# Kernel tuning notes

Measured on AMD Instinct MI355X. Metric: run time of the kernel, lower is better.

## Reference

```python
import jax, jax.numpy as jnp
import numpy as np

DEPTH = 9
NUM_LEAVES = 2 ** DEPTH            # 512
NUM_BRANCHES = 2 ** DEPTH - 1      # 511


def _leaf_paths(depth):
    """For each leaf, the BFS (heap-order) branch indices along its root->leaf
    path and the left/right bit taken at each branch (1 = right)."""
    L = 2 ** depth
    idx = np.zeros((L, depth), np.int32)
    bits = np.zeros((L, depth), np.int32)
    for l in range(L):
        node = 0
        for t in range(depth):
            b = (l >> (depth - 1 - t)) & 1
            idx[l, t] = node
            bits[l, t] = b
            node = 2 * node + 1 + b
    return jnp.asarray(idx), jnp.asarray(bits)

PATH_IDX, PATH_BITS = _leaf_paths(DEPTH)


def setup_inputs() -> dict:
    key = jax.random.key(0)
    k1, k2, k3 = jax.random.split(key, 3)
    B, D, W, H = 128, 256, 28, 28
    C = 200
    return {
        "xs": jax.random.normal(k1, (B, D, W, H), jnp.float32),
        "prototypes": jax.random.normal(k2, (NUM_BRANCHES, D, 1, 1), jnp.float32),
        "leaf_params": jax.random.normal(k3, (NUM_LEAVES, C), jnp.float32),
    }


def reference(xs, prototypes, leaf_params):
    # ---- L2Conv2D: squared-L2 distance map via conv decomposition ----
    B, D, W, H = xs.shape
    P = prototypes.shape[0]
    p = prototypes.reshape(P, D)                       # W1 = H1 = 1
    x2 = jnp.sum(xs * xs, axis=1)                      # [B, W, H]
    p2 = jnp.sum(p * p, axis=1)                        # [P]
    xp = jnp.einsum('bdwh,pd->bpwh', xs, p)            # [B, P, W, H]
    sq = x2[:, None] - 2.0 * xp + p2[None, :, None, None]
    distances = jnp.sqrt(jnp.abs(sq) + 1e-14)          # [B, P, W, H]

    # ---- min-pool over full spatial extent (avg-pool unused: focal off) ----
    min_distances = jnp.min(distances, axis=(2, 3))    # [B, P]
    similarities = jnp.exp(-min_distances)             # [B, P], ps per branch

    # ---- soft tree routing: pa(leaf) = prod over path of ps / (1-ps) ----
    ps_path = similarities[:, PATH_IDX]                # [B, L, depth]
    step = jnp.where(PATH_BITS[None] == 1, ps_path, 1.0 - ps_path)
    pa = jnp.prod(step, axis=-1)                       # [B, L]

    # ---- mix leaf class distributions (distributed sampling strategy) ----
    ds = jax.nn.softmax(leaf_params, axis=-1)          # [L, C]
    return pa @ ds                                     # [B, C]
```

## Files before the change

kernel.cpp:

```cpp
#include <hip/hip_runtime.h>
#include <hip/hip_bf16.h>

typedef __attribute__((ext_vector_type(8))) short bf16x8;
typedef __attribute__((ext_vector_type(4))) float f32x4;

#define D_K    256
#define WH     784
#define WHH    392
#define P_REAL 511
#define P_PAD  512
#define C_OUT  200
#define NLEAF  512
#define TDEPTH 9

#define NT      32
#define NTILES  13
#define TILE_USH 8192

#define WS_PB   0
#define WS_P2   262144
#define WS_DS   264192
#define WS_PM   673792

static __device__ __forceinline__ unsigned short f2bf(float x) {
    union { float f; unsigned int u; } v; v.f = x;
    unsigned int r = v.u + 0x7FFFu + ((v.u >> 16) & 1u);
    return (unsigned short)(r >> 16);
}

__global__ __launch_bounds__(64)
void prep2_kernel(const float* __restrict__ protos, const float* __restrict__ lp,
                  unsigned short* __restrict__ pb, float* __restrict__ p2,
                  float* __restrict__ ds) {
    int bid = blockIdx.x;
    int l = threadIdx.x;
    if (bid < P_PAD) {
        int p = bid;
        f32x4 v = {0.f, 0.f, 0.f, 0.f};
        if (p < P_REAL)
            v = *reinterpret_cast<const f32x4*>(protos + (size_t)p * D_K + 4 * l);
        ushort4 w;
        w.x = f2bf(-2.f * v[0]); w.y = f2bf(-2.f * v[1]);
        w.z = f2bf(-2.f * v[2]); w.w = f2bf(-2.f * v[3]);
        *reinterpret_cast<ushort4*>(pb + (size_t)p * D_K + 4 * l) = w;
        float s = v[0]*v[0] + v[1]*v[1] + v[2]*v[2] + v[3]*v[3];
#pragma unroll
        for (int m = 32; m >= 1; m >>= 1) s += __shfl_xor(s, m, 64);
        if (l == 0) p2[p] = s;
    } else {
        int row = bid - P_PAD;
        float v[4];
        float mx = -3.4e38f;
#pragma unroll
        for (int i = 0; i < 4; ++i) {
            int c = l + 64 * i;
            v[i] = (c < C_OUT) ? lp[(size_t)row * C_OUT + c] : -3.4e38f;
            mx = fmaxf(mx, v[i]);
        }
#pragma unroll
        for (int m = 32; m >= 1; m >>= 1) mx = fmaxf(mx, __shfl_xor(mx, m, 64));
        float sum = 0.f;
#pragma unroll
        for (int i = 0; i < 4; ++i) {
            int c = l + 64 * i;
            if (c < C_OUT) { v[i] = expf(v[i] - mx); sum += v[i]; }
        }
#pragma unroll
        for (int m = 32; m >= 1; m >>= 1) sum += __shfl_xor(sum, m, 64);
        float inv = 1.f / sum;
#pragma unroll
        for (int i = 0; i < 4; ++i) {
            int c = l + 64 * i;
            if (c < C_OUT) ds[(size_t)row * C_OUT + c] = v[i] * inv;
        }
    }
}

__global__ __launch_bounds__(512, 2)
void proto_min_kernel(const float* __restrict__ xs,
                      const unsigned short* __restrict__ pb,
                      float* __restrict__ pm) {
    __shared__ unsigned short Xs[2][TILE_USH];
    __shared__ float x2buf[2][8*68 + 8];

    const int tid  = threadIdx.x;
    const int wv   = tid >> 6;
    const int lane = tid & 63;
    const int g    = lane >> 4;
    const int lr   = lane & 15;

    const int b   = blockIdx.x >> 1;
    const int whh = blockIdx.x & 1;

    const float* xb = xs + (size_t)b * (D_K * WH) + whh * WHH;

    bf16x8 af[4][8];
#pragma unroll
    for (int mf = 0; mf < 4; ++mf) {
        const unsigned short* rp = pb + (size_t)(64*wv + 16*mf + lr) * D_K + 8*g;
#pragma unroll
        for (int ks = 0; ks < 8; ++ks)
            af[mf][ks] = *reinterpret_cast<const bf16x8*>(rp + 32*ks);
    }

    const int n4 = tid & 7;
    const int kq = tid >> 3;

    float rmin[4][4];
#pragma unroll
    for (int mf = 0; mf < 4; ++mf)
#pragma unroll
        for (int r = 0; r < 4; ++r) rmin[mf][r] = 3.0e38f;

    f32x4 ld[4];

#define LOAD_TILE(T) do {                                                     \
        int colb = (T) * NT + 4 * n4;                                         \
        if (colb > WHH - 4) colb = WHH - 4;                                   \
        const float* rowp = xb + (size_t)(4*kq) * WH + colb;                  \
        _Pragma("unroll")                                                     \
        for (int r = 0; r < 4; ++r)                                           \
            ld[r] = *reinterpret_cast<const f32x4*>(rowp + r * WH);           \
    } while (0)

#define STAGE_TILE(DST) do {                                                  \
        f32x4 x2a = {0.f, 0.f, 0.f, 0.f};                                     \
        _Pragma("unroll")                                                     \
        for (int r = 0; r < 4; ++r) {                                         \
            f32x4 v = ld[r];                                                  \
            x2a[0] += v[0]*v[0]; x2a[1] += v[1]*v[1];                         \
            x2a[2] += v[2]*v[2]; x2a[3] += v[3]*v[3];                         \
        }                                                                     \
        _Pragma("unroll")                                                     \
        for (int c = 0; c < 4; ++c) {                                         \
            int n = 4*n4 + c;                                                 \
            float2 f01 = make_float2(ld[0][c], ld[1][c]);                     \
            float2 f23 = make_float2(ld[2][c], ld[3][c]);                     \
            __hip_bfloat162 b01 = __float22bfloat162_rn(f01);                 \
            __hip_bfloat162 b23 = __float22bfloat162_rn(f23);                 \
            uint2 w;                                                          \
            w.x = *reinterpret_cast<unsigned int*>(&b01);                     \
            w.y = *reinterpret_cast<unsigned int*>(&b23);                     \
            int off = n*256 + (((kq >> 1) ^ (n & 7)) << 3) + ((kq & 1) << 2); \
            *reinterpret_cast<uint2*>(&Xs[DST][off]) = w;                     \
        }                                                                     \
        _Pragma("unroll")                                                     \
        for (int c = 0; c < 4; ++c) {                                         \
            x2a[c] += __shfl_xor(x2a[c], 8, 64);                              \
            x2a[c] += __shfl_xor(x2a[c], 16, 64);                             \
            x2a[c] += __shfl_xor(x2a[c], 32, 64);                             \
        }                                                                     \
        if (lane < 8) {                                                       \
            _Pragma("unroll")                                                 \
            for (int c = 0; c < 4; ++c)                                       \
                x2buf[DST][lane*68 + c*8 + wv] = x2a[c];                      \
        }                                                                     \
    } while (0)

#define X2_READ(NF, OUT) do {                                                 \
        int n = 16*(NF) + lr;                                                 \
        const float* xp = &x2buf[buf][(n >> 2)*68 + (n & 3)*8];               \
        f32x4 q0 = *reinterpret_cast<const f32x4*>(xp);                       \
        f32x4 q1 = *reinterpret_cast<const f32x4*>(xp + 4);                   \
        OUT = ((q0[0]+q0[1]) + (q0[2]+q0[3]))                                 \
            + ((q1[0]+q1[1]) + (q1[2]+q1[3]));                                \
    } while (0)

#define BURST(NF, ACC) do {                                                   \
        __builtin_amdgcn_s_setprio(1);                                        \
        _Pragma("unroll")                                                     \
        for (int ks = 0; ks < 8; ++ks) {                                      \
            int n = 16*(NF) + lr;                                             \
            int off = n*256 + ((((ks << 2) + g) ^ (n & 7)) << 3);             \
            bf16x8 bfr = *reinterpret_cast<const bf16x8*>(&Xs[buf][off]);     \
            _Pragma("unroll")                                                 \
            for (int mf = 0; mf < 4; ++mf)                                    \
                ACC[mf] = __builtin_amdgcn_mfma_f32_16x16x32_bf16(            \
                    af[mf][ks], bfr, ACC[mf], 0, 0, 0);                       \
        }                                                                     \
        __builtin_amdgcn_s_setprio(0);                                        \
    } while (0)

#define MIN_UPD(ACC) do {                                                     \
        _Pragma("unroll")                                                     \
        for (int mf = 0; mf < 4; ++mf)                                        \
            _Pragma("unroll")                                                 \
            for (int r = 0; r < 4; ++r)                                       \
                rmin[mf][r] = fminf(rmin[mf][r], ACC[mf][r]);                 \
    } while (0)

    LOAD_TILE(0);
    STAGE_TILE(0);
    __syncthreads();

    int buf = 0;
    f32x4 acc0[4], acc1[4];

    for (int t = 0; t < NTILES - 1; ++t) {
        LOAD_TILE(t + 1);

        float x2v0; X2_READ(0, x2v0);
#pragma unroll
        for (int mf = 0; mf < 4; ++mf)
            acc0[mf] = (f32x4){x2v0, x2v0, x2v0, x2v0};

        BURST(0, acc0);
        MIN_UPD(acc0);

        STAGE_TILE(buf ^ 1);

        float x2v1; X2_READ(1, x2v1);
#pragma unroll
        for (int mf = 0; mf < 4; ++mf)
            acc1[mf] = (f32x4){x2v1, x2v1, x2v1, x2v1};

        BURST(1, acc1);
        MIN_UPD(acc1);

        __syncthreads();
        buf ^= 1;
    }

    {
        float x2v0; X2_READ(0, x2v0);
#pragma unroll
        for (int mf = 0; mf < 4; ++mf)
            acc0[mf] = (f32x4){x2v0, x2v0, x2v0, x2v0};
        BURST(0, acc0);
        MIN_UPD(acc0);

        float x2v1; X2_READ(1, x2v1);
#pragma unroll
        for (int mf = 0; mf < 4; ++mf)
            acc1[mf] = (f32x4){x2v1, x2v1, x2v1, x2v1};
        BURST(1, acc1);
        MIN_UPD(acc1);
    }

#pragma unroll
    for (int mf = 0; mf < 4; ++mf)
#pragma unroll
        for (int r = 0; r < 4; ++r) {
            float v = rmin[mf][r];
#pragma unroll
            for (int m = 1; m <= 8; m <<= 1)
                v = fminf(v, __shfl_xor(v, m, 64));
            rmin[mf][r] = v;
        }

    if (lr == 0) {
        float* pmw = pm + ((size_t)b * 2 + whh) * P_PAD;
#pragma unroll
        for (int mf = 0; mf < 4; ++mf)
#pragma unroll
            for (int r = 0; r < 4; ++r)
                pmw[64*wv + 16*mf + 4*g + r] = rmin[mf][r];
    }
#undef LOAD_TILE
#undef STAGE_TILE
#undef X2_READ
#undef BURST
#undef MIN_UPD
}

__global__ __launch_bounds__(256)
void out_kernel(const float* __restrict__ pm, const float* __restrict__ p2,
                const float* __restrict__ ds, float* __restrict__ out) {
    __shared__ float sim[NLEAF];
    __shared__ float pa[NLEAF];
    int b = blockIdx.x;
    int t = threadIdx.x;
    const float* pm0 = pm + (size_t)b * 2 * P_PAD;
#pragma unroll
    for (int j = 0; j < 2; ++j) {
        int p = t + 256 * j;
        float m = fminf(pm0[p], pm0[P_PAD + p]);
        float sq = m + p2[p];
        sim[p] = expf(-sqrtf(fabsf(sq) + 1e-14f));
    }
    __syncthreads();
#pragma unroll
    for (int j = 0; j < 2; ++j) {
        int leaf = t + 256 * j;
        int node = 0;
        float prod = 1.f;
#pragma unroll
        for (int st = 0; st < TDEPTH; ++st) {
            int bit = (leaf >> (TDEPTH - 1 - st)) & 1;
            float sv = sim[node];
            prod *= bit ? sv : (1.f - sv);
            node = 2 * node + 1 + bit;
        }
        pa[leaf] = prod;
    }
    __syncthreads();
    if (t < C_OUT) {
        float a0 = 0.f, a1 = 0.f, a2 = 0.f, a3 = 0.f;
        for (int l = 0; l < NLEAF; l += 4) {
            a0 += pa[l + 0] * ds[(size_t)(l + 0) * C_OUT + t];
            a1 += pa[l + 1] * ds[(size_t)(l + 1) * C_OUT + t];
            a2 += pa[l + 2] * ds[(size_t)(l + 2) * C_OUT + t];
            a3 += pa[l + 3] * ds[(size_t)(l + 3) * C_OUT + t];
        }
        out[(size_t)b * C_OUT + t] = (a0 + a1) + (a2 + a3);
    }
}

extern "C" void kernel_launch(void* const* d_in, const int* in_sizes, int n_in,
                              void* d_out, int out_size, void* d_ws, size_t ws_size,
                              hipStream_t stream) {
    (void)in_sizes; (void)n_in; (void)out_size; (void)ws_size;
    const float* xs     = (const float*)d_in[0];
    const float* protos = (const float*)d_in[1];
    const float* lp     = (const float*)d_in[2];
    float* out = (float*)d_out;

    char* ws = (char*)d_ws;
    unsigned short* pb = (unsigned short*)(ws + WS_PB);
    float* p2   = (float*)(ws + WS_P2);
    float* dsm  = (float*)(ws + WS_DS);
    float* pm   = (float*)(ws + WS_PM);

    prep2_kernel<<<1024, 64, 0, stream>>>(protos, lp, pb, p2, dsm);
    proto_min_kernel<<<256, 512, 0, stream>>>(xs, pb, pm);
    out_kernel<<<128, 256, 0, stream>>>(pm, p2, dsm, out);
}
```

Baseline: 58.47 us.

## Deepen global-load prefetch to two tiles ahead and change LDS swizzle key

Replaces the single register staging buffer with two (ldA/ldB) so global loads for tile t+2/t+3 are issued two tiles ahead of use. The main loop is unrolled by two so the LDS buffer indices are compile-time constants. It also changes the XOR swizzle key for the bf16 tile in shared memory to (n ^ n>>2)&7, aiming to reduce bank conflicts on stores and reads. The deeper prefetch hides more global-memory latency at the cost of extra VGPRs, which may lower occupancy.

```diff
diff --git a/kernel.cpp b/kernel.cpp
--- a/kernel.cpp
+++ b/kernel.cpp
@@ -112,36 +112,37 @@
 #pragma unroll
         for (int r = 0; r < 4; ++r) rmin[mf][r] = 3.0e38f;
 
-    f32x4 ld[4];
-
-#define LOAD_TILE(T) do {                                                     \
+    f32x4 ldA[4], ldB[4];
+
+#define LOAD_T(T, LD) do {                                                    \
         int colb = (T) * NT + 4 * n4;                                         \
         if (colb > WHH - 4) colb = WHH - 4;                                   \
         const float* rowp = xb + (size_t)(4*kq) * WH + colb;                  \
         _Pragma("unroll")                                                     \
         for (int r = 0; r < 4; ++r)                                           \
-            ld[r] = *reinterpret_cast<const f32x4*>(rowp + r * WH);           \
-    } while (0)
-
-#define STAGE_TILE(DST) do {                                                  \
+            LD[r] = *reinterpret_cast<const f32x4*>(rowp + r * WH);           \
+    } while (0)
+
+#define STAGE_T(DST, LD) do {                                                 \
         f32x4 x2a = {0.f, 0.f, 0.f, 0.f};                                     \
         _Pragma("unroll")                                                     \
         for (int r = 0; r < 4; ++r) {                                         \
-            f32x4 v = ld[r];                                                  \
+            f32x4 v = LD[r];                                                  \
             x2a[0] += v[0]*v[0]; x2a[1] += v[1]*v[1];                         \
             x2a[2] += v[2]*v[2]; x2a[3] += v[3]*v[3];                         \
         }                                                                     \
         _Pragma("unroll")                                                     \
         for (int c = 0; c < 4; ++c) {                                         \
             int n = 4*n4 + c;                                                 \
-            float2 f01 = make_float2(ld[0][c], ld[1][c]);                     \
-            float2 f23 = make_float2(ld[2][c], ld[3][c]);                     \
+            int key = (n ^ n4) & 7;                                           \
+            float2 f01 = make_float2(LD[0][c], LD[1][c]);                     \
+            float2 f23 = make_float2(LD[2][c], LD[3][c]);                     \
             __hip_bfloat162 b01 = __float22bfloat162_rn(f01);                 \
             __hip_bfloat162 b23 = __float22bfloat162_rn(f23);                 \
             uint2 w;                                                          \
             w.x = *reinterpret_cast<unsigned int*>(&b01);                     \
             w.y = *reinterpret_cast<unsigned int*>(&b23);                     \
-            int off = n*256 + (((kq >> 1) ^ (n & 7)) << 3) + ((kq & 1) << 2); \
+            int off = n*256 + (((kq >> 1) ^ key) << 3) + ((kq & 1) << 2);     \
             *reinterpret_cast<uint2*>(&Xs[DST][off]) = w;                     \
         }                                                                     \
         _Pragma("unroll")                                                     \
@@ -157,22 +158,23 @@
         }                                                                     \
     } while (0)
 
-#define X2_READ(NF, OUT) do {                                                 \
+#define X2_READ(BUF, NF, OUT) do {                                            \
         int n = 16*(NF) + lr;                                                 \
-        const float* xp = &x2buf[buf][(n >> 2)*68 + (n & 3)*8];               \
+        const float* xp = &x2buf[BUF][(n >> 2)*68 + (n & 3)*8];               \
         f32x4 q0 = *reinterpret_cast<const f32x4*>(xp);                       \
         f32x4 q1 = *reinterpret_cast<const f32x4*>(xp + 4);                   \
         OUT = ((q0[0]+q0[1]) + (q0[2]+q0[3]))                                 \
             + ((q1[0]+q1[1]) + (q1[2]+q1[3]));                                \
     } while (0)
 
-#define BURST(NF, ACC) do {                                                   \
+#define BURST(BUF, NF, ACC) do {                                              \
         __builtin_amdgcn_s_setprio(1);                                        \
         _Pragma("unroll")                                                     \
         for (int ks = 0; ks < 8; ++ks) {                                      \
             int n = 16*(NF) + lr;                                             \
-            int off = n*256 + ((((ks << 2) + g) ^ (n & 7)) << 3);             \
-            bf16x8 bfr = *reinterpret_cast<const bf16x8*>(&Xs[buf][off]);     \
+            int key = (n ^ (n >> 2)) & 7;                                     \
+            int off = n*256 + (((((ks) << 2) + g) ^ key) << 3);               \
+            bf16x8 bfr = *reinterpret_cast<const bf16x8*>(&Xs[BUF][off]);     \
             _Pragma("unroll")                                                 \
             for (int mf = 0; mf < 4; ++mf)                                    \
                 ACC[mf] = __builtin_amdgcn_mfma_f32_16x16x32_bf16(            \
@@ -189,52 +191,51 @@
                 rmin[mf][r] = fminf(rmin[mf][r], ACC[mf][r]);                 \
     } while (0)
 
-    LOAD_TILE(0);
-    STAGE_TILE(0);
+#define TILE_BODY(T, CUR, NXT, LD) do {                                       \
+        f32x4 acc[4];                                                         \
+        float x2v0; X2_READ(CUR, 0, x2v0);                                    \
+        _Pragma("unroll")                                                     \
+        for (int mf = 0; mf < 4; ++mf)                                        \
+            acc[mf] = (f32x4){x2v0, x2v0, x2v0, x2v0};                        \
+        BURST(CUR, 0, acc);                                                   \
+        MIN_UPD(acc);                                                         \
+        STAGE_T(NXT, LD);                                                     \
+        if ((T) + 3 < NTILES) LOAD_T((T) + 3, LD);                            \
+        float x2v1; X2_READ(CUR, 1, x2v1);                                    \
+        _Pragma("unroll")                                                     \
+        for (int mf = 0; mf < 4; ++mf)                                        \
+            acc[mf] = (f32x4){x2v1, x2v1, x2v1, x2v1};                        \
+        BURST(CUR, 1, acc);                                                   \
+        MIN_UPD(acc);                                                         \
+        __syncthreads();                                                      \
+    } while (0)
+
+    LOAD_T(0, ldA);
+    STAGE_T(0, ldA);
+    LOAD_T(1, ldA);
+    LOAD_T(2, ldB);
     __syncthreads();
 
-    int buf = 0;
-    f32x4 acc0[4], acc1[4];
-
-    for (int t = 0; t < NTILES - 1; ++t) {
-        LOAD_TILE(t + 1);
-
-        float x2v0; X2_READ(0, x2v0);
+    for (int tt = 0; tt < 6; ++tt) {
+        const int t0 = 2 * tt;
+        TILE_BODY(t0,     0, 1, ldA);
+        TILE_BODY(t0 + 1, 1, 0, ldB);
+    }
+
+    {
+        f32x4 acc[4];
+        float x2v0; X2_READ(0, 0, x2v0);
 #pragma unroll
         for (int mf = 0; mf < 4; ++mf)
-            acc0[mf] = (f32x4){x2v0, x2v0, x2v0, x2v0};
-
-        BURST(0, acc0);
-        MIN_UPD(acc0);
-
-        STAGE_TILE(buf ^ 1);
-
-        float x2v1; X2_READ(1, x2v1);
+            acc[mf] = (f32x4){x2v0, x2v0, x2v0, x2v0};
+        BURST(0, 0, acc);
+        MIN_UPD(acc);
+        float x2v1; X2_READ(0, 1, x2v1);
 #pragma unroll
         for (int mf = 0; mf < 4; ++mf)
-            acc1[mf] = (f32x4){x2v1, x2v1, x2v1, x2v1};
-
-        BURST(1, acc1);
-        MIN_UPD(acc1);
-
-        __syncthreads();
-        buf ^= 1;
-    }
-
-    {
-        float x2v0; X2_READ(0, x2v0);
-#pragma unroll
-        for (int mf = 0; mf < 4; ++mf)
-            acc0[mf] = (f32x4){x2v0, x2v0, x2v0, x2v0};
-        BURST(0, acc0);
-        MIN_UPD(acc0);
-
-        float x2v1; X2_READ(1, x2v1);
-#pragma unroll
-        for (int mf = 0; mf < 4; ++mf)
-            acc1[mf] = (f32x4){x2v1, x2v1, x2v1, x2v1};
-        BURST(1, acc1);
-        MIN_UPD(acc1);
+            acc[mf] = (f32x4){x2v1, x2v1, x2v1, x2v1};
+        BURST(0, 1, acc);
+        MIN_UPD(acc);
     }
 
 #pragma unroll
@@ -256,11 +257,12 @@
             for (int r = 0; r < 4; ++r)
                 pmw[64*wv + 16*mf + 4*g + r] = rmin[mf][r];
     }
-#undef LOAD_TILE
-#undef STAGE_TILE
+#undef LOAD_T
+#undef STAGE_T
 #undef X2_READ
 #undef BURST
 #undef MIN_UPD
+#undef TILE_BODY
 }
 
 __global__ __launch_bounds__(256)
```

Result: slower. 74.74 us (+27.8%).

## Double spatial tile width and interleave half-tile staging with MFMA steps

Applied to the files above, without the earlier changes.

The proto_min kernel's spatial tile grows from 32 to 64 columns, so the loop runs 7 times instead of 13 and needs fewer block barriers. Each tile is loaded and staged in two 32-column halves, each placed between pairs of MFMA bursts, to overlap global loads and LDS writes with compute. The LDS swizzle key changes to (n ^ n>>2) & 7 to suit the wider tile. In exchange, LDS use per block roughly doubles, which could limit co-residency, and more of the clamped tail columns are duplicated work.

```diff
diff --git a/kernel.cpp b/kernel.cpp
--- a/kernel.cpp
+++ b/kernel.cpp
@@ -13,9 +13,9 @@
 #define NLEAF  512
 #define TDEPTH 9
 
-#define NT      32
-#define NTILES  13
-#define TILE_USH 8192
+#define NT      64
+#define NTILES  7
+#define TILE_USH (64*256)
 
 #define WS_PB   0
 #define WS_P2   262144
@@ -81,7 +81,7 @@
                       const unsigned short* __restrict__ pb,
                       float* __restrict__ pm) {
     __shared__ unsigned short Xs[2][TILE_USH];
-    __shared__ float x2buf[2][8*68 + 8];
+    __shared__ float x2buf[2][16*68 + 8];
 
     const int tid  = threadIdx.x;
     const int wv   = tid >> 6;
@@ -114,8 +114,8 @@
 
     f32x4 ld[4];
 
-#define LOAD_TILE(T) do {                                                     \
-        int colb = (T) * NT + 4 * n4;                                         \
+#define LOAD_H(T, H) do {                                                     \
+        int colb = (T) * NT + 32*(H) + 4 * n4;                                \
         if (colb > WHH - 4) colb = WHH - 4;                                   \
         const float* rowp = xb + (size_t)(4*kq) * WH + colb;                  \
         _Pragma("unroll")                                                     \
@@ -123,7 +123,7 @@
             ld[r] = *reinterpret_cast<const f32x4*>(rowp + r * WH);           \
     } while (0)
 
-#define STAGE_TILE(DST) do {                                                  \
+#define STAGE_H(H, DST) do {                                                  \
         f32x4 x2a = {0.f, 0.f, 0.f, 0.f};                                     \
         _Pragma("unroll")                                                     \
         for (int r = 0; r < 4; ++r) {                                         \
@@ -133,7 +133,8 @@
         }                                                                     \
         _Pragma("unroll")                                                     \
         for (int c = 0; c < 4; ++c) {                                         \
-            int n = 4*n4 + c;                                                 \
+            int n = 32*(H) + 4*n4 + c;                                        \
+            int key = (n ^ (n >> 2)) & 7;                                     \
             float2 f01 = make_float2(ld[0][c], ld[1][c]);                     \
             float2 f23 = make_float2(ld[2][c], ld[3][c]);                     \
             __hip_bfloat162 b01 = __float22bfloat162_rn(f01);                 \
@@ -141,7 +142,7 @@
             uint2 w;                                                          \
             w.x = *reinterpret_cast<unsigned int*>(&b01);                     \
             w.y = *reinterpret_cast<unsigned int*>(&b23);                     \
-            int off = n*256 + (((kq >> 1) ^ (n & 7)) << 3) + ((kq & 1) << 2); \
+            int off = n*256 + (((kq >> 1) ^ key) << 3) + ((kq & 1) << 2);     \
             *reinterpret_cast<uint2*>(&Xs[DST][off]) = w;                     \
         }                                                                     \
         _Pragma("unroll")                                                     \
@@ -153,26 +154,27 @@
         if (lane < 8) {                                                       \
             _Pragma("unroll")                                                 \
             for (int c = 0; c < 4; ++c)                                       \
-                x2buf[DST][lane*68 + c*8 + wv] = x2a[c];                      \
-        }                                                                     \
-    } while (0)
-
-#define X2_READ(NF, OUT) do {                                                 \
+                x2buf[DST][(8*(H) + lane)*68 + c*8 + wv] = x2a[c];            \
+        }                                                                     \
+    } while (0)
+
+#define X2_READ(BUF, NF, OUT) do {                                            \
         int n = 16*(NF) + lr;                                                 \
-        const float* xp = &x2buf[buf][(n >> 2)*68 + (n & 3)*8];               \
+        const float* xp = &x2buf[BUF][(n >> 2)*68 + (n & 3)*8];               \
         f32x4 q0 = *reinterpret_cast<const f32x4*>(xp);                       \
         f32x4 q1 = *reinterpret_cast<const f32x4*>(xp + 4);                   \
         OUT = ((q0[0]+q0[1]) + (q0[2]+q0[3]))                                 \
             + ((q1[0]+q1[1]) + (q1[2]+q1[3]));                                \
     } while (0)
 
-#define BURST(NF, ACC) do {                                                   \
+#define BURST(BUF, NF, ACC) do {                                              \
         __builtin_amdgcn_s_setprio(1);                                        \
         _Pragma("unroll")                                                     \
         for (int ks = 0; ks < 8; ++ks) {                                      \
             int n = 16*(NF) + lr;                                             \
-            int off = n*256 + ((((ks << 2) + g) ^ (n & 7)) << 3);             \
-            bf16x8 bfr = *reinterpret_cast<const bf16x8*>(&Xs[buf][off]);     \
+            int key = (n ^ (n >> 2)) & 7;                                     \
+            int off = n*256 + (((((ks) << 2) + g) ^ key) << 3);               \
+            bf16x8 bfr = *reinterpret_cast<const bf16x8*>(&Xs[BUF][off]);     \
             _Pragma("unroll")                                                 \
             for (int mf = 0; mf < 4; ++mf)                                    \
                 ACC[mf] = __builtin_amdgcn_mfma_f32_16x16x32_bf16(            \
@@ -181,60 +183,46 @@
         __builtin_amdgcn_s_setprio(0);                                        \
     } while (0)
 
-#define MIN_UPD(ACC) do {                                                     \
+#define NF_STEP(BUF, NF) do {                                                 \
+        f32x4 acc[4];                                                         \
+        float x2v; X2_READ(BUF, NF, x2v);                                     \
+        _Pragma("unroll")                                                     \
+        for (int mf = 0; mf < 4; ++mf)                                        \
+            acc[mf] = (f32x4){x2v, x2v, x2v, x2v};                            \
+        BURST(BUF, NF, acc);                                                  \
         _Pragma("unroll")                                                     \
         for (int mf = 0; mf < 4; ++mf)                                        \
             _Pragma("unroll")                                                 \
             for (int r = 0; r < 4; ++r)                                       \
-                rmin[mf][r] = fminf(rmin[mf][r], ACC[mf][r]);                 \
-    } while (0)
-
-    LOAD_TILE(0);
-    STAGE_TILE(0);
+                rmin[mf][r] = fminf(rmin[mf][r], acc[mf][r]);                 \
+    } while (0)
+
+    LOAD_H(0, 0); STAGE_H(0, 0);
+    LOAD_H(0, 1); STAGE_H(1, 0);
     __syncthreads();
 
     int buf = 0;
-    f32x4 acc0[4], acc1[4];
-
-    for (int t = 0; t < NTILES - 1; ++t) {
-        LOAD_TILE(t + 1);
-
-        float x2v0; X2_READ(0, x2v0);
-#pragma unroll
-        for (int mf = 0; mf < 4; ++mf)
-            acc0[mf] = (f32x4){x2v0, x2v0, x2v0, x2v0};
-
-        BURST(0, acc0);
-        MIN_UPD(acc0);
-
-        STAGE_TILE(buf ^ 1);
-
-        float x2v1; X2_READ(1, x2v1);
-#pragma unroll
-        for (int mf = 0; mf < 4; ++mf)
-            acc1[mf] = (f32x4){x2v1, x2v1, x2v1, x2v1};
-
-        BURST(1, acc1);
-        MIN_UPD(acc1);
-
-        __syncthreads();
+    for (int t = 0; t < NTILES; ++t) {
+        const bool more = (t + 1 < NTILES);
+
+        if (more) LOAD_H(t + 1, 0);
+
+        NF_STEP(buf, 0);
+        NF_STEP(buf, 1);
+
+        if (more) {
+            STAGE_H(0, buf ^ 1);
+            LOAD_H(t + 1, 1);
+        }
+
+        NF_STEP(buf, 2);
+        NF_STEP(buf, 3);
+
+        if (more) {
+            STAGE_H(1, buf ^ 1);
+            __syncthreads();
+        }
         buf ^= 1;
-    }
-
-    {
-        float x2v0; X2_READ(0, x2v0);
-#pragma unroll
-        for (int mf = 0; mf < 4; ++mf)
-            acc0[mf] = (f32x4){x2v0, x2v0, x2v0, x2v0};
-        BURST(0, acc0);
-        MIN_UPD(acc0);
-
-        float x2v1; X2_READ(1, x2v1);
-#pragma unroll
-        for (int mf = 0; mf < 4; ++mf)
-            acc1[mf] = (f32x4){x2v1, x2v1, x2v1, x2v1};
-        BURST(1, acc1);
-        MIN_UPD(acc1);
     }
 
 #pragma unroll
@@ -256,11 +244,11 @@
             for (int r = 0; r < 4; ++r)
                 pmw[64*wv + 16*mf + 4*g + r] = rmin[mf][r];
     }
-#undef LOAD_TILE
-#undef STAGE_TILE
+#undef LOAD_H
+#undef STAGE_H
 #undef X2_READ
 #undef BURST
-#undef MIN_UPD
+#undef NF_STEP
 }
 
 __global__ __launch_bounds__(256)
```

Measured after the change: 125.7 us. 2.15x slower.
